# Kernel tuning notes

Measured on AMD Instinct MI355X. Metric: run time of the kernel, lower is better.

## Reference

```python
import jax, jax.numpy as jnp
import numpy as np

B, S, H, NH = 1, 2048, 2048, 16
HD = H // NH
EPS = 1e-5
NEG = jnp.finfo(jnp.float32).min


def _alibi_slopes(n_heads):
    # standard Bloom alibi slopes (n_heads power of 2)
    start = 2.0 ** (-(2.0 ** -(np.log2(n_heads) - 3)))
    return start * (start ** np.arange(n_heads))


def setup_inputs() -> dict:
    key = jax.random.key(0)
    ks = jax.random.split(key, 10)
    s = 0.02
    hidden_states = jax.random.normal(ks[0], (B, S, H), jnp.float32)
    # causal mask: True = masked (future positions)
    causal = ~jnp.tril(jnp.ones((S, S), dtype=bool))
    attention_mask = causal[None, None, :, :]  # [1,1,S,S]
    # alibi bias [B*NH, 1, S]
    slopes = jnp.asarray(_alibi_slopes(NH), jnp.float32)  # [NH]
    pos = jnp.arange(S, dtype=jnp.float32)
    alibi = (slopes[:, None] * pos[None, :])[:, None, :]  # [NH,1,S]
    alibi = jnp.tile(alibi, (B, 1, 1))  # [B*NH,1,S]
    return {
        "hidden_states": hidden_states,
        "attention_mask": attention_mask,
        "alibi": alibi,
        "head_mask": 0,
        "ln1_g": jnp.ones((H,), jnp.float32),
        "ln1_b": jnp.zeros((H,), jnp.float32),
        "qkv_w": jax.random.normal(ks[1], (3 * H, H), jnp.float32) * s,
        "qkv_b": jnp.zeros((3 * H,), jnp.float32),
        "dense_w": jax.random.normal(ks[2], (H, H), jnp.float32) * s,
        "dense_b": jnp.zeros((H,), jnp.float32),
        "ln2_g": jnp.ones((H,), jnp.float32),
        "ln2_b": jnp.zeros((H,), jnp.float32),
        "fc1_w": jax.random.normal(ks[3], (4 * H, H), jnp.float32) * s,
        "fc1_b": jnp.zeros((4 * H,), jnp.float32),
        "fc2_w": jax.random.normal(ks[4], (H, 4 * H), jnp.float32) * s,
        "fc2_b": jnp.zeros((H,), jnp.float32),
    }


def _ln(x, g, b):
    mu = jnp.mean(x, axis=-1, keepdims=True)
    var = jnp.mean(jnp.square(x - mu), axis=-1, keepdims=True)
    return (x - mu) * jax.lax.rsqrt(var + EPS) * g + b


def _gelu(x):
    # Bloom tanh-approx GELU
    return x * 0.5 * (1.0 + jnp.tanh(0.79788456 * x * (1.0 + 0.044715 * x * x)))


def reference(hidden_states, attention_mask, alibi, head_mask,
              ln1_g, ln1_b, qkv_w, qkv_b, dense_w, dense_b,
              ln2_g, ln2_b, fc1_w, fc1_b, fc2_w, fc2_b):
    b, s, h = hidden_states.shape
    x = _ln(hidden_states, ln1_g, ln1_b)
    residual = hidden_states  # apply_residual_connection_post_layernorm=False

    qkv = x @ qkv_w.T + qkv_b                      # [b,s,3H]
    qkv = qkv.reshape(b, s, NH, 3, HD)             # per-head interleaved
    q, k, v = qkv[..., 0, :], qkv[..., 1, :], qkv[..., 2, :]  # [b,s,nh,hd]

    inv = 1.0 / jnp.sqrt(jnp.float32(HD))
    scores = jnp.einsum('bqnd,bknd->bnqk', q, k) * inv  # [b,nh,s,s]
    scores = scores + alibi.reshape(b, NH, 1, s)
    scores = jnp.where(attention_mask, NEG, scores)
    w = jax.nn.softmax(scores, axis=-1)
    # head_mask == 0 -> falsy in original; no head masking applied
    ctx = jnp.einsum('bnqk,bknd->bqnd', w, v).reshape(b, s, h)
    attn_out = ctx @ dense_w.T + dense_b + residual

    y = _ln(attn_out, ln2_g, ln2_b)
    residual2 = attn_out
    hdn = _gelu(y @ fc1_w.T + fc1_b)
    out = hdn @ fc2_w.T + fc2_b + residual2
    return out
```

## Files before the change

kernel.cpp:

```cpp
#include <hip/hip_runtime.h>
#include <hip/hip_bf16.h>

#define SQ 2048
#define HH 2048
#define NHEAD 16
#define HD 128
#define QKVW (NHEAD*3*HD)

typedef __attribute__((ext_vector_type(8))) short bf16x8;
typedef __attribute__((ext_vector_type(4))) float f32x4;
typedef __attribute__((ext_vector_type(16))) float f32x16;

__device__ inline unsigned short f2bf(float f) {
    union { float f; unsigned u; } x; x.f = f;
    unsigned r = x.u + 0x7FFFu + ((x.u >> 16) & 1u);
    return (unsigned short)(r >> 16);
}

__device__ inline unsigned pack_bf2(float a, float b) {
    return (unsigned)f2bf(a) | ((unsigned)f2bf(b) << 16);
}

__device__ inline float gelu_f(float x) {
    float x3 = x * (1.f + 0.044715f * x * x);
    return 0.5f * x * (1.f + tanhf(0.79788456f * x3));
}

__device__ inline void gld16(void* lds, const void* g) {
    __builtin_amdgcn_global_load_lds(
        (__attribute__((address_space(1))) void*)(g),
        (__attribute__((address_space(3))) void*)(lds), 16, 0, 0);
}

__global__ __launch_bounds__(256) void cvt_kernel(
    const float* __restrict__ in, unsigned short* __restrict__ out, int n4)
{
    int i = blockIdx.x * blockDim.x + threadIdx.x;
    int stride = gridDim.x * blockDim.x;
    for (; i < n4; i += stride) {
        float4 f = ((const float4*)in)[i];
        ushort4 o;
        o.x = f2bf(f.x); o.y = f2bf(f.y); o.z = f2bf(f.z); o.w = f2bf(f.w);
        ((ushort4*)out)[i] = o;
    }
}

__global__ __launch_bounds__(256) void ln_kernel(
    const float* __restrict__ in, const float* __restrict__ g,
    const float* __restrict__ b, unsigned short* __restrict__ out)
{
    int row = blockIdx.x;
    int t = threadIdx.x, lane = t & 63, wid = t >> 6;
    const float4* rp = (const float4*)(in + (size_t)row * HH);
    float4 v0 = rp[t], v1 = rp[t + 256];
    float s  = v0.x + v0.y + v0.z + v0.w + v1.x + v1.y + v1.z + v1.w;
    float ss = v0.x*v0.x + v0.y*v0.y + v0.z*v0.z + v0.w*v0.w
             + v1.x*v1.x + v1.y*v1.y + v1.z*v1.z + v1.w*v1.w;
    #pragma unroll
    for (int o = 32; o; o >>= 1) { s += __shfl_down(s, o); ss += __shfl_down(ss, o); }
    __shared__ float r0[4], r1[4];
    if (lane == 0) { r0[wid] = s; r1[wid] = ss; }
    __syncthreads();
    s  = r0[0] + r0[1] + r0[2] + r0[3];
    ss = r1[0] + r1[1] + r1[2] + r1[3];
    float mu = s * (1.f / HH);
    float var = ss * (1.f / HH) - mu * mu;
    float rs = rsqrtf(var + 1e-5f);
    float4 g0 = ((const float4*)g)[t], g1 = ((const float4*)g)[t + 256];
    float4 b0 = ((const float4*)b)[t], b1 = ((const float4*)b)[t + 256];
    ushort4 o0, o1;
    o0.x = f2bf((v0.x - mu) * rs * g0.x + b0.x);
    o0.y = f2bf((v0.y - mu) * rs * g0.y + b0.y);
    o0.z = f2bf((v0.z - mu) * rs * g0.z + b0.z);
    o0.w = f2bf((v0.w - mu) * rs * g0.w + b0.w);
    o1.x = f2bf((v1.x - mu) * rs * g1.x + b1.x);
    o1.y = f2bf((v1.y - mu) * rs * g1.y + b1.y);
    o1.z = f2bf((v1.z - mu) * rs * g1.z + b1.z);
    o1.w = f2bf((v1.w - mu) * rs * g1.w + b1.w);
    ushort4* op = (ushort4*)(out + (size_t)row * HH);
    op[t] = o0; op[t + 256] = o1;
}

template<int NP>
__global__ __launch_bounds__(256) void reduceN_kernel(
    const float* __restrict__ p0, const float* __restrict__ p1,
    const float* __restrict__ p2, const float* __restrict__ p3,
    const float* __restrict__ res, const float* __restrict__ bias,
    float* __restrict__ out, int n4, int nc4m1)
{
    int i = blockIdx.x * blockDim.x + threadIdx.x;
    int st = gridDim.x * blockDim.x;
    for (; i < n4; i += st) {
        float4 a = ((const float4*)p0)[i];
        float4 b = ((const float4*)p1)[i];
        float4 r = ((const float4*)res)[i];
        float4 bv = ((const float4*)bias)[i & nc4m1];
        float4 o;
        o.x = a.x + b.x + r.x + bv.x;
        o.y = a.y + b.y + r.y + bv.y;
        o.z = a.z + b.z + r.z + bv.z;
        o.w = a.w + b.w + r.w + bv.w;
        if (NP >= 3) {
            float4 c = ((const float4*)p2)[i];
            o.x += c.x; o.y += c.y; o.z += c.z; o.w += c.w;
        }
        if (NP >= 4) {
            float4 d = ((const float4*)p3)[i];
            o.x += d.x; o.y += d.y; o.z += d.z; o.w += d.w;
        }
        ((float4*)out)[i] = o;
    }
}


template<int MODE, int GELU_ON>
__global__ __launch_bounds__(256, 4) void gemm128(
    const unsigned short* __restrict__ A, const unsigned short* __restrict__ B,
    const float* __restrict__ bias, void* __restrict__ outp,
    unsigned short* __restrict__ vtb, void* __restrict__ outp_hi,
    int N, int lda, int ldb, int kLen, int Ktot, int CH, int CW)
{
    __shared__ __align__(16) unsigned short Asm[2][128][32];
    __shared__ __align__(16) unsigned short Bsm[2][128][32];

    int t = threadIdx.x, lane = t & 63, wid = t >> 6;
    int lo = lane & 15, hi = lane >> 4;
    int wr = wid >> 1, wc = wid & 1;

    int id = (blockIdx.z * gridDim.y + blockIdx.y) * gridDim.x + blockIdx.x;
    int xcd = id & 7, local = id >> 3;
    int cgx = gridDim.x / CW;
    int cr = xcd / cgx, cc = xcd - cr * cgx;
    int lr = local / CW, lc = local - lr * CW;
    int R  = cr * CH + lr;
    int bn = cc * CW + lc;
    int bm = R % gridDim.y;
    int bz = R / gridDim.y;
    int m0 = bm * 128, n0 = bn * 128;
    int kstart = bz * kLen;
    int rem = Ktot - kstart;
    int nt = ((rem < kLen) ? rem : kLen) >> 5;

    int rS = t >> 2, cS = t & 3;
    int sc0_ = (cS ^ (rS & 3)) << 3;
    const unsigned short* Ab = A + (size_t)m0 * lda + kstart;
    const unsigned short* Bb = B + (size_t)n0 * ldb + kstart;
    const unsigned short* Asrc0 = Ab + (size_t)rS * lda + sc0_;
    const unsigned short* Asrc1 = Ab + (size_t)(64 + rS) * lda + sc0_;
    const unsigned short* Bsrc0 = Bb + (size_t)rS * ldb + sc0_;
    const unsigned short* Bsrc1 = Bb + (size_t)(64 + rS) * ldb + sc0_;

    gld16(&Asm[0][wid * 16][0], Asrc0);
    gld16(&Asm[0][64 + wid * 16][0], Asrc1);
    gld16(&Bsm[0][wid * 16][0], Bsrc0);
    gld16(&Bsm[0][64 + wid * 16][0], Bsrc1);
    __syncthreads();

    f32x4 acc[4][4] = {};
    for (int u = 0; u < nt; u++) {
        int buf = u & 1, nbuf = buf ^ 1;
        int t1 = ((u + 1 < nt) ? u + 1 : nt - 1) * 32;
        gld16(&Asm[nbuf][wid * 16][0], Asrc0 + t1);
        gld16(&Asm[nbuf][64 + wid * 16][0], Asrc1 + t1);
        gld16(&Bsm[nbuf][wid * 16][0], Bsrc0 + t1);
        gld16(&Bsm[nbuf][64 + wid * 16][0], Bsrc1 + t1);
        __builtin_amdgcn_s_setprio(1);
        {
            bf16x8 af[4], bfr[4];
            #pragma unroll
            for (int i = 0; i < 4; i++) {
                int r = wr * 64 + i * 16 + lo;
                af[i] = *(const bf16x8*)&Asm[buf][r][(hi ^ (r & 3)) << 3];
            }
            #pragma unroll
            for (int c = 0; c < 4; c++) {
                int r = wc * 64 + c * 16 + lo;
                bfr[c] = *(const bf16x8*)&Bsm[buf][r][(hi ^ (r & 3)) << 3];
            }
            #pragma unroll
            for (int i = 0; i < 4; i++)
                #pragma unroll
                for (int c = 0; c < 4; c++)
                    acc[i][c] = __builtin_amdgcn_mfma_f32_16x16x32_bf16(
                        bfr[c], af[i], acc[i][c], 0, 0, 0);
        }
        __builtin_amdgcn_s_setprio(0);
        __syncthreads();
    }

    if (MODE == 0) {
        float* po;
        if (bz == 0)      po = (float*)outp;
        else if (bz == 1) po = (float*)outp + (size_t)SQ * N;
        else if (bz == 2) po = (float*)outp_hi;
        else              po = (float*)vtb;
        #pragma unroll
        for (int i = 0; i < 4; i++) {
            int gr = m0 + wr * 64 + i * 16 + lo;
            #pragma unroll
            for (int c = 0; c < 4; c++) {
                int gc = n0 + wc * 64 + c * 16 + hi * 4;
                *(f32x4*)&po[(size_t)gr * N + gc] = acc[i][c];
            }
        }
    } else if (MODE == 1) {
        unsigned short* op = (unsigned short*)outp;
        #pragma unroll
        for (int i = 0; i < 4; i++) {
            int gr = m0 + wr * 64 + i * 16 + lo;
            #pragma unroll
            for (int c = 0; c < 4; c++) {
                int gc = n0 + wc * 64 + c * 16 + hi * 4;
                float4 bi = *(const float4*)&bias[gc];
                float v0 = acc[i][c][0] + bi.x, v1 = acc[i][c][1] + bi.y;
                float v2 = acc[i][c][2] + bi.z, v3 = acc[i][c][3] + bi.w;
                if (GELU_ON) { v0 = gelu_f(v0); v1 = gelu_f(v1); v2 = gelu_f(v2); v3 = gelu_f(v3); }
                ushort4 o; o.x = f2bf(v0); o.y = f2bf(v1); o.z = f2bf(v2); o.w = f2bf(v3);
                *(ushort4*)&op[(size_t)gr * N + gc] = o;
            }
        }
    } else {
        unsigned short* op = (unsigned short*)outp;
        int head = n0 / 384;
        int cat = (n0 >> 7) % 3;
        #pragma unroll
        for (int i = 0; i < 4; i++) {
            int gr = m0 + wr * 64 + i * 16 + lo;
            #pragma unroll
            for (int c = 0; c < 4; c++) {
                int gc = n0 + wc * 64 + c * 16 + hi * 4;
                float4 bi = *(const float4*)&bias[gc];
                float v0 = acc[i][c][0] + bi.x, v1 = acc[i][c][1] + bi.y;
                float v2 = acc[i][c][2] + bi.z, v3 = acc[i][c][3] + bi.w;
                if (cat == 2) {
                    int d = wc * 64 + c * 16 + hi * 4;
                    unsigned short* vp = vtb + (size_t)(head * HD + d) * SQ + gr;
                    vp[0]      = f2bf(v0);
                    vp[SQ]     = f2bf(v1);
                    vp[2 * SQ] = f2bf(v2);
                    vp[3 * SQ] = f2bf(v3);
                } else {
                    ushort4 o; o.x = f2bf(v0); o.y = f2bf(v1); o.z = f2bf(v2); o.w = f2bf(v3);
                    *(ushort4*)&op[(size_t)gr * N + gc] = o;
                }
            }
        }
    }
}

__global__ __launch_bounds__(128) void attn_kernel(
    const unsigned short* __restrict__ qkvB,
    const unsigned short* __restrict__ vtb,
    unsigned short* __restrict__ ctx)
{
    int w = blockIdx.x;
    int lid = (w & 7) * 64 + (w >> 3);
    int n = lid >> 5, qt = lid & 31;
    int t = threadIdx.x, lane = t & 63, wid = t >> 6;
    int l32 = lane & 31, h2 = lane >> 5;
    int q0 = qt * 64, qg = q0 + wid * 32 + l32;

    __shared__ __align__(16) unsigned short Ks[64][128];
    __shared__ __align__(16) unsigned short Vt[128][64];

    bf16x8 qf[8];
    const unsigned short* qp = qkvB + (size_t)qg * QKVW + n * 384 + h2 * 8;
    #pragma unroll
    for (int d8 = 0; d8 < 8; d8++)
        qf[d8] = *(const bf16x8*)(qp + d8 * 16);

    const float slope = exp2f(-0.5f * (float)(n + 1));
    const float inv = 0.08838834764831845f;
    float m = -INFINITY, lsum = 0.f;
    f32x16 ao[4] = {};

    int krow = lane >> 4, kch = lane & 15;
    int vrow = lane >> 3, vch = lane & 7;
    const unsigned short* kb_ = qkvB + n * 384 + 128;
    const unsigned short* vb_ = vtb + (size_t)n * HD * SQ;
    const char* ksb = (const char*)&Ks[0][0];
    const char* vsb = (const char*)&Vt[0][0];

    int nkb = qt + 1;
    for (int kb = 0; kb < nkb; kb++) {
        int k0 = kb * 64;
        __syncthreads();
        #pragma unroll
        for (int s = 0; s < 8; s++) {
            int r = wid * 32 + s * 4 + krow;
            gld16(&Ks[wid * 32 + s * 4][0],
                  kb_ + (size_t)(k0 + r) * QKVW + ((kch ^ (r & 7)) << 3));
            int dd = wid * 64 + s * 8 + vrow;
            gld16(&Vt[wid * 64 + s * 8][0],
                  vb_ + (size_t)dd * SQ + k0 + ((vch ^ (dd & 7)) << 3));
        }
        __syncthreads();

        f32x16 sc0 = {}, sc1 = {};
        #pragma unroll
        for (int d8 = 0; d8 < 8; d8++) {
            int ch = ((d8 * 2 + h2) ^ (l32 & 7)) << 4;
            bf16x8 kf0 = *(const bf16x8*)(ksb + l32 * 256 + ch);
            bf16x8 kf1 = *(const bf16x8*)(ksb + (32 + l32) * 256 + ch);
            sc0 = __builtin_amdgcn_mfma_f32_32x32x16_bf16(kf0, qf[d8], sc0, 0, 0, 0);
            sc1 = __builtin_amdgcn_mfma_f32_32x32x16_bf16(kf1, qf[d8], sc1, 0, 0, 0);
        }

        float tmax = -INFINITY;
        int last = (kb == nkb - 1);
        #pragma unroll
        for (int r = 0; r < 16; r++) {
            int kl = (r & 3) + 8 * (r >> 2) + 4 * h2;
            float s0 = sc0[r] * inv + slope * (float)(k0 + kl);
            float s1 = sc1[r] * inv + slope * (float)(k0 + 32 + kl);
            if (last) {
                if (k0 + kl > qg) s0 = -INFINITY;
                if (k0 + 32 + kl > qg) s1 = -INFINITY;
            }
            sc0[r] = s0; sc1[r] = s1;
            tmax = fmaxf(tmax, fmaxf(s0, s1));
        }
        tmax = fmaxf(tmax, __shfl_xor(tmax, 32));
        if (!__all(tmax <= m + 8.f)) {
            float mnew = fmaxf(m, tmax);
            float sca = __expf(m - mnew);
            m = mnew;
            lsum *= sca;
            #pragma unroll
            for (int db = 0; db < 4; db++)
                #pragma unroll
                for (int e = 0; e < 16; e++) ao[db][e] *= sca;
        }
        float psum = 0.f;
        #pragma unroll
        for (int r = 0; r < 16; r++) {
            sc0[r] = __expf(sc0[r] - m); psum += sc0[r];
            sc1[r] = __expf(sc1[r] - m); psum += sc1[r];
        }
        psum += __shfl_xor(psum, 32);
        lsum += psum;

        #pragma unroll
        for (int kstep = 0; kstep < 4; kstep++) {
            const int ks1 = kstep & 1;
            float a0, a1, a2, a3, b0, b1, b2, b3;
            if (kstep < 2) {
                a0 = sc0[8*ks1+0]; a1 = sc0[8*ks1+1]; a2 = sc0[8*ks1+2]; a3 = sc0[8*ks1+3];
                b0 = sc0[8*ks1+4]; b1 = sc0[8*ks1+5]; b2 = sc0[8*ks1+6]; b3 = sc0[8*ks1+7];
            } else {
                a0 = sc1[8*ks1+0]; a1 = sc1[8*ks1+1]; a2 = sc1[8*ks1+2]; a3 = sc1[8*ks1+3];
                b0 = sc1[8*ks1+4]; b1 = sc1[8*ks1+5]; b2 = sc1[8*ks1+6]; b3 = sc1[8*ks1+7];
            }
            unsigned ku0 = pack_bf2(h2 ? b0 : a0, h2 ? b1 : a1);
            unsigned ku1 = pack_bf2(h2 ? b2 : a2, h2 ? b3 : a3);
            unsigned su0 = pack_bf2(h2 ? a0 : b0, h2 ? a1 : b1);
            unsigned su1 = pack_bf2(h2 ? a2 : b2, h2 ? a3 : b3);
            unsigned r0 = (unsigned)__shfl_xor((int)su0, 32);
            unsigned r1 = (unsigned)__shfl_xor((int)su1, 32);
            union { int4 i; bf16x8 v; } u;
            u.i.x = h2 ? (int)r0  : (int)ku0;
            u.i.y = h2 ? (int)r1  : (int)ku1;
            u.i.z = h2 ? (int)ku0 : (int)r0;
            u.i.w = h2 ? (int)ku1 : (int)r1;
            bf16x8 pf = u.v;
            int ch = ((kstep * 2 + h2) ^ (l32 & 7)) << 4;
            #pragma unroll
            for (int db = 0; db < 4; db++) {
                bf16x8 vf = *(const bf16x8*)(vsb + (db * 32 + l32) * 128 + ch);
                ao[db] = __builtin_amdgcn_mfma_f32_32x32x16_bf16(vf, pf, ao[db], 0, 0, 0);
            }
        }
    }

    float rl = 1.f / lsum;
    #pragma unroll
    for (int db = 0; db < 4; db++)
        #pragma unroll
        for (int g = 0; g < 4; g++) {
            ushort4 o;
            o.x = f2bf(ao[db][g*4+0] * rl);
            o.y = f2bf(ao[db][g*4+1] * rl);
            o.z = f2bf(ao[db][g*4+2] * rl);
            o.w = f2bf(ao[db][g*4+3] * rl);
            *(ushort4*)(ctx + (size_t)qg * HH + n * HD + db * 32 + g * 8 + h2 * 4) = o;
        }
}

extern "C" void kernel_launch(void* const* d_in, const int* in_sizes, int n_in,
                              void* d_out, int out_size, void* d_ws, size_t ws_size,
                              hipStream_t stream) {
    const float* hs    = (const float*)d_in[0];
    const float* ln1g  = (const float*)d_in[4];
    const float* ln1b  = (const float*)d_in[5];
    const float* qkvw  = (const float*)d_in[6];
    const float* qkvb  = (const float*)d_in[7];
    const float* dw    = (const float*)d_in[8];
    const float* db    = (const float*)d_in[9];
    const float* ln2g  = (const float*)d_in[10];
    const float* ln2b  = (const float*)d_in[11];
    const float* f1w   = (const float*)d_in[12];
    const float* f1b   = (const float*)d_in[13];
    const float* f2w   = (const float*)d_in[14];
    const float* f2b   = (const float*)d_in[15];
    float* out = (float*)d_out;

    char* ws = (char*)d_ws;
    size_t off = 0;
    auto alloc = [&](size_t nbytes) {
        void* p = ws + off; off += (nbytes + 255) & ~(size_t)255; return p;
    };
    unsigned short* xbf  = (unsigned short*)alloc((size_t)SQ * HH * 2);
    unsigned short* qkvB = (unsigned short*)alloc((size_t)SQ * QKVW * 2);
    unsigned short* vtB  = (unsigned short*)alloc((size_t)NHEAD * HD * SQ * 2);
    unsigned short* ctx  = (unsigned short*)alloc((size_t)SQ * HH * 2);
    float*          attn = (float*)alloc((size_t)SQ * HH * 4);
    unsigned short* y    = (unsigned short*)alloc((size_t)SQ * HH * 2);
    unsigned short* hdn  = (unsigned short*)alloc((size_t)SQ * 4 * HH * 2);
    unsigned short* wbuf = (unsigned short*)alloc((size_t)4 * HH * HH * 2);

    const size_t PQ = (size_t)SQ * HH;
    float* part = (float*)ws;

    ln_kernel<<<SQ, 256, 0, stream>>>(hs, ln1g, ln1b, xbf);

    cvt_kernel<<<2048, 256, 0, stream>>>(qkvw, wbuf, QKVW * HH / 4);
    gemm128<2, 0><<<dim3(QKVW / 128, SQ / 128, 1), 256, 0, stream>>>(
        xbf, wbuf, qkvb, qkvB, vtB, nullptr, QKVW, HH, HH, HH, HH, 8, 12);

    attn_kernel<<<512, 128, 0, stream>>>(qkvB, vtB, ctx);

    cvt_kernel<<<1024, 256, 0, stream>>>(dw, wbuf, HH * HH / 4);
    gemm128<0, 0><<<dim3(HH / 128, SQ / 128, 4), 256, 0, stream>>>(
        ctx, wbuf, nullptr, part, (unsigned short*)((float*)hdn + PQ), hdn,
        HH, HH, HH, HH / 4, HH, 16, 8);
    reduceN_kernel<4><<<2048, 256, 0, stream>>>(
        part, part + PQ, (float*)hdn, (float*)hdn + PQ, hs, db, attn, SQ * HH / 4, HH / 4 - 1);

    ln_kernel<<<SQ, 256, 0, stream>>>(attn, ln2g, ln2b, y);

    cvt_kernel<<<2048, 256, 0, stream>>>(f1w, wbuf, 4 * HH * HH / 4);
    gemm128<1, 1><<<dim3(4 * HH / 128, SQ / 128, 1), 256, 0, stream>>>(
        y, wbuf, f1b, hdn, nullptr, nullptr, 4 * HH, HH, HH, HH, HH, 8, 16);

    cvt_kernel<<<2048, 256, 0, stream>>>(f2w, wbuf, 4 * HH * HH / 4);
    gemm128<0, 0><<<dim3(HH / 128, SQ / 128, 3), 256, 0, stream>>>(
        hdn, wbuf, nullptr, part, nullptr, part + 2 * PQ,
        HH, 4 * HH, 4 * HH, 2752, 4 * HH, 12, 8);
    reduceN_kernel<3><<<2048, 256, 0, stream>>>(
        part, part + PQ, part + 2 * PQ, nullptr, attn, f2b, out, SQ * HH / 4, HH / 4 - 1);
}
```

Baseline: 446.2 us.

## Use 256x256-tile 1024-thread GEMM for MLP layers and change LDS swizzle

Adds a gemm1024 kernel that uses 256x256 output tiles with 16 waves per block, and switches the FC1 and FC2 GEMMs to it. FC2 moves from a 3-way to a 4-way split-K, with the fourth partial written into the output buffer and reduced in place. The LDS XOR swizzle in both GEMMs now keys on (row>>1)&3 instead of row&3, to cut bank conflicts on the fragment reads. Larger tiles give more operand reuse per block, at the cost of fewer blocks and possibly lower occupancy, since launch_bounds(1024,4) is unlikely to hold with 64 KB of LDS per block.

Result: no change. 444.2 us (-0.4%).

```diff
diff --git a/kernel.cpp b/kernel.cpp
--- a/kernel.cpp
+++ b/kernel.cpp
@@ -112,7 +112,6 @@
     }
 }
 
-
 template<int MODE, int GELU_ON>
 __global__ __launch_bounds__(256, 4) void gemm128(
     const unsigned short* __restrict__ A, const unsigned short* __restrict__ B,
@@ -142,13 +141,14 @@
     int nt = ((rem < kLen) ? rem : kLen) >> 5;
 
     int rS = t >> 2, cS = t & 3;
-    int sc0_ = (cS ^ (rS & 3)) << 3;
+    int scA0 = (cS ^ ((rS >> 1) & 3)) << 3;
+    int scA1 = (cS ^ (((64 + rS) >> 1) & 3)) << 3;
     const unsigned short* Ab = A + (size_t)m0 * lda + kstart;
     const unsigned short* Bb = B + (size_t)n0 * ldb + kstart;
-    const unsigned short* Asrc0 = Ab + (size_t)rS * lda + sc0_;
-    const unsigned short* Asrc1 = Ab + (size_t)(64 + rS) * lda + sc0_;
-    const unsigned short* Bsrc0 = Bb + (size_t)rS * ldb + sc0_;
-    const unsigned short* Bsrc1 = Bb + (size_t)(64 + rS) * ldb + sc0_;
+    const unsigned short* Asrc0 = Ab + (size_t)rS * lda + scA0;
+    const unsigned short* Asrc1 = Ab + (size_t)(64 + rS) * lda + scA1;
+    const unsigned short* Bsrc0 = Bb + (size_t)rS * ldb + scA0;
+    const unsigned short* Bsrc1 = Bb + (size_t)(64 + rS) * ldb + scA1;
 
     gld16(&Asm[0][wid * 16][0], Asrc0);
     gld16(&Asm[0][64 + wid * 16][0], Asrc1);
@@ -170,12 +170,12 @@
             #pragma unroll
             for (int i = 0; i < 4; i++) {
                 int r = wr * 64 + i * 16 + lo;
-                af[i] = *(const bf16x8*)&Asm[buf][r][(hi ^ (r & 3)) << 3];
+                af[i] = *(const bf16x8*)&Asm[buf][r][(hi ^ ((r >> 1) & 3)) << 3];
             }
             #pragma unroll
             for (int c = 0; c < 4; c++) {
                 int r = wc * 64 + c * 16 + lo;
-                bfr[c] = *(const bf16x8*)&Bsm[buf][r][(hi ^ (r & 3)) << 3];
+                bfr[c] = *(const bf16x8*)&Bsm[buf][r][(hi ^ ((r >> 1) & 3)) << 3];
             }
             #pragma unroll
             for (int i = 0; i < 4; i++)
@@ -243,6 +243,104 @@
                     ushort4 o; o.x = f2bf(v0); o.y = f2bf(v1); o.z = f2bf(v2); o.w = f2bf(v3);
                     *(ushort4*)&op[(size_t)gr * N + gc] = o;
                 }
+            }
+        }
+    }
+}
+
+template<int MODE, int GELU_ON>
+__global__ __launch_bounds__(1024, 4) void gemm1024(
+    const unsigned short* __restrict__ A, const unsigned short* __restrict__ B,
+    const float* __restrict__ bias, void* __restrict__ outp,
+    void* __restrict__ outp_hi,
+    int N, int lda, int ldb, int kLen, int Ktot, int CH, int CW)
+{
+    __shared__ __align__(16) unsigned short Asm[2][256][32];
+    __shared__ __align__(16) unsigned short Bsm[2][256][32];
+
+    int t = threadIdx.x, lane = t & 63, wid = t >> 6;
+    int lo = lane & 15, hi = lane >> 4;
+    int wr = wid >> 2, wc = wid & 3;
+
+    int id = (blockIdx.z * gridDim.y + blockIdx.y) * gridDim.x + blockIdx.x;
+    int xcd = id & 7, local = id >> 3;
+    int cgx = gridDim.x / CW;
+    int cr = xcd / cgx, cc = xcd - cr * cgx;
+    int lr = local / CW, lc = local - lr * CW;
+    int R  = cr * CH + lr;
+    int bn = cc * CW + lc;
+    int bm = R % gridDim.y;
+    int bz = R / gridDim.y;
+    int m0 = bm * 256, n0 = bn * 256;
+    int kstart = bz * kLen;
+    int rem = Ktot - kstart;
+    int nt = ((rem < kLen) ? rem : kLen) >> 5;
+
+    int rS = t >> 2, cS = t & 3;
+    int scS = (cS ^ ((rS >> 1) & 3)) << 3;
+    const unsigned short* Asrc = A + (size_t)(m0 + rS) * lda + kstart + scS;
+    const unsigned short* Bsrc = B + (size_t)(n0 + rS) * ldb + kstart + scS;
+
+    gld16(&Asm[0][wid * 16][0], Asrc);
+    gld16(&Bsm[0][wid * 16][0], Bsrc);
+    __syncthreads();
+
+    f32x4 acc[4][4] = {};
+    for (int u = 0; u < nt; u++) {
+        int buf = u & 1, nbuf = buf ^ 1;
+        int t1 = ((u + 1 < nt) ? u + 1 : nt - 1) * 32;
+        gld16(&Asm[nbuf][wid * 16][0], Asrc + t1);
+        gld16(&Bsm[nbuf][wid * 16][0], Bsrc + t1);
+        __builtin_amdgcn_s_setprio(1);
+        {
+            bf16x8 af[4], bfr[4];
+            #pragma unroll
+            for (int i = 0; i < 4; i++) {
+                int r = wr * 64 + i * 16 + lo;
+                af[i] = *(const bf16x8*)&Asm[buf][r][(hi ^ ((r >> 1) & 3)) << 3];
+            }
+            #pragma unroll
+            for (int c = 0; c < 4; c++) {
+                int r = wc * 64 + c * 16 + lo;
+                bfr[c] = *(const bf16x8*)&Bsm[buf][r][(hi ^ ((r >> 1) & 3)) << 3];
+            }
+            #pragma unroll
+            for (int i = 0; i < 4; i++)
+                #pragma unroll
+                for (int c = 0; c < 4; c++)
+                    acc[i][c] = __builtin_amdgcn_mfma_f32_16x16x32_bf16(
+                        bfr[c], af[i], acc[i][c], 0, 0, 0);
+        }
+        __builtin_amdgcn_s_setprio(0);
+        __syncthreads();
+    }
+
+    if (MODE == 0) {
+        float* po = (bz < 3) ? (float*)outp + (size_t)bz * SQ * N
+                             : (float*)outp_hi;
+        #pragma unroll
+        for (int i = 0; i < 4; i++) {
+            int gr = m0 + wr * 64 + i * 16 + lo;
+            #pragma unroll
+            for (int c = 0; c < 4; c++) {
+                int gc = n0 + wc * 64 + c * 16 + hi * 4;
+                *(f32x4*)&po[(size_t)gr * N + gc] = acc[i][c];
+            }
+        }
+    } else {
+        unsigned short* op = (unsigned short*)outp;
+        #pragma unroll
+        for (int i = 0; i < 4; i++) {
+            int gr = m0 + wr * 64 + i * 16 + lo;
+            #pragma unroll
+            for (int c = 0; c < 4; c++) {
+                int gc = n0 + wc * 64 + c * 16 + hi * 4;
+                float4 bi = *(const float4*)&bias[gc];
+                float v0 = acc[i][c][0] + bi.x, v1 = acc[i][c][1] + bi.y;
+                float v2 = acc[i][c][2] + bi.z, v3 = acc[i][c][3] + bi.w;
+                if (GELU_ON) { v0 = gelu_f(v0); v1 = gelu_f(v1); v2 = gelu_f(v2); v3 = gelu_f(v3); }
+                ushort4 o; o.x = f2bf(v0); o.y = f2bf(v1); o.z = f2bf(v2); o.w = f2bf(v3);
+                *(ushort4*)&op[(size_t)gr * N + gc] = o;
             }
         }
     }
@@ -439,13 +537,12 @@
     ln_kernel<<<SQ, 256, 0, stream>>>(attn, ln2g, ln2b, y);
 
     cvt_kernel<<<2048, 256, 0, stream>>>(f1w, wbuf, 4 * HH * HH / 4);
-    gemm128<1, 1><<<dim3(4 * HH / 128, SQ / 128, 1), 256, 0, stream>>>(
-        y, wbuf, f1b, hdn, nullptr, nullptr, 4 * HH, HH, HH, HH, HH, 8, 16);
+    gemm1024<1, 1><<<dim3(4 * HH / 256, SQ / 256, 1), 1024, 0, stream>>>(
+        y, wbuf, f1b, hdn, nullptr, 4 * HH, HH, HH, HH, HH, 4, 8);
 
     cvt_kernel<<<2048, 256, 0, stream>>>(f2w, wbuf, 4 * HH * HH / 4);
-    gemm128<0, 0><<<dim3(HH / 128, SQ / 128, 3), 256, 0, stream>>>(
-        hdn, wbuf, nullptr, part, nullptr, part + 2 * PQ,
-        HH, 4 * HH, 4 * HH, 2752, 4 * HH, 12, 8);
-    reduceN_kernel<3><<<2048, 256, 0, stream>>>(
-        part, part + PQ, part + 2 * PQ, nullptr, attn, f2b, out, SQ * HH / 4, HH / 4 - 1);
-}
+    gemm1024<0, 0><<<dim3(HH / 256, SQ / 256, 4), 1024, 0, stream>>>(
+        hdn, wbuf, nullptr, part, out, HH, 4 * HH, 4 * HH, HH, 4 * HH, 8, 4);
+    reduceN_kernel<4><<<2048, 256, 0, stream>>>(
+        part, part + PQ, part + 2 * PQ, out, attn, f2b, out, SQ * HH / 4, HH / 4 - 1);
+}
```

## Switch GEMMs to 256x256 tiles with 1024-thread blocks and K=64 steps

Applied to the files above, without the earlier changes.

Replaces the 128x128, 256-thread GEMM with a 256x256 output tile computed by 16 waves, a K-step of 64 with an 8-way XOR swizzle in LDS, and retuned grid and chunking parameters. Each block reuses more data per tile, which cuts redundant global and L2 traffic for the A and B panels. The fc2 split-K changes from 3 to 4 chunks, with the fourth partial written into the output buffer and reduced in place. The cost is fewer blocks per GEMM, 128 KB of LDS per block that limits occupancy, and a larger wave count for each barrier to synchronise.

New measurement: 415.7 us. 1.07x faster.

```diff
diff --git a/kernel.cpp b/kernel.cpp
--- a/kernel.cpp
+++ b/kernel.cpp
@@ -112,20 +112,20 @@
     }
 }
 
-
 template<int MODE, int GELU_ON>
-__global__ __launch_bounds__(256, 4) void gemm128(
+__global__ __launch_bounds__(1024, 4) void gemm1024(
     const unsigned short* __restrict__ A, const unsigned short* __restrict__ B,
     const float* __restrict__ bias, void* __restrict__ outp,
     unsigned short* __restrict__ vtb, void* __restrict__ outp_hi,
+    void* __restrict__ outp_hi2,
     int N, int lda, int ldb, int kLen, int Ktot, int CH, int CW)
 {
-    __shared__ __align__(16) unsigned short Asm[2][128][32];
-    __shared__ __align__(16) unsigned short Bsm[2][128][32];
+    __shared__ __align__(16) unsigned short Asm[2][256][64];
+    __shared__ __align__(16) unsigned short Bsm[2][256][64];
 
     int t = threadIdx.x, lane = t & 63, wid = t >> 6;
     int lo = lane & 15, hi = lane >> 4;
-    int wr = wid >> 1, wc = wid & 1;
+    int wr = wid >> 2, wc = wid & 3;
 
     int id = (blockIdx.z * gridDim.y + blockIdx.y) * gridDim.x + blockIdx.x;
     int xcd = id & 7, local = id >> 3;
@@ -136,46 +136,46 @@
     int bn = cc * CW + lc;
     int bm = R % gridDim.y;
     int bz = R / gridDim.y;
-    int m0 = bm * 128, n0 = bn * 128;
+    int m0 = bm * 256, n0 = bn * 256;
     int kstart = bz * kLen;
     int rem = Ktot - kstart;
-    int nt = ((rem < kLen) ? rem : kLen) >> 5;
-
-    int rS = t >> 2, cS = t & 3;
-    int sc0_ = (cS ^ (rS & 3)) << 3;
-    const unsigned short* Ab = A + (size_t)m0 * lda + kstart;
-    const unsigned short* Bb = B + (size_t)n0 * ldb + kstart;
-    const unsigned short* Asrc0 = Ab + (size_t)rS * lda + sc0_;
-    const unsigned short* Asrc1 = Ab + (size_t)(64 + rS) * lda + sc0_;
-    const unsigned short* Bsrc0 = Bb + (size_t)rS * ldb + sc0_;
-    const unsigned short* Bsrc1 = Bb + (size_t)(64 + rS) * ldb + sc0_;
-
-    gld16(&Asm[0][wid * 16][0], Asrc0);
-    gld16(&Asm[0][64 + wid * 16][0], Asrc1);
-    gld16(&Bsm[0][wid * 16][0], Bsrc0);
-    gld16(&Bsm[0][64 + wid * 16][0], Bsrc1);
+    int nt = ((rem < kLen) ? rem : kLen) >> 6;
+
+    int rS = t >> 3, cS = t & 7;
+    int scS = (cS ^ (rS & 7)) << 3;
+    const unsigned short* Asrc0 = A + (size_t)(m0 + rS) * lda + kstart + scS;
+    const unsigned short* Asrc1 = A + (size_t)(m0 + 128 + rS) * lda + kstart + scS;
+    const unsigned short* Bsrc0 = B + (size_t)(n0 + rS) * ldb + kstart + scS;
+    const unsigned short* Bsrc1 = B + (size_t)(n0 + 128 + rS) * ldb + kstart + scS;
+
+    gld16(&Asm[0][wid * 8][0], Asrc0);
+    gld16(&Asm[0][128 + wid * 8][0], Asrc1);
+    gld16(&Bsm[0][wid * 8][0], Bsrc0);
+    gld16(&Bsm[0][128 + wid * 8][0], Bsrc1);
     __syncthreads();
 
     f32x4 acc[4][4] = {};
     for (int u = 0; u < nt; u++) {
         int buf = u & 1, nbuf = buf ^ 1;
-        int t1 = ((u + 1 < nt) ? u + 1 : nt - 1) * 32;
-        gld16(&Asm[nbuf][wid * 16][0], Asrc0 + t1);
-        gld16(&Asm[nbuf][64 + wid * 16][0], Asrc1 + t1);
-        gld16(&Bsm[nbuf][wid * 16][0], Bsrc0 + t1);
-        gld16(&Bsm[nbuf][64 + wid * 16][0], Bsrc1 + t1);
+        int t1 = ((u + 1 < nt) ? u + 1 : nt - 1) * 64;
+        gld16(&Asm[nbuf][wid * 8][0], Asrc0 + t1);
+        gld16(&Asm[nbuf][128 + wid * 8][0], Asrc1 + t1);
+        gld16(&Bsm[nbuf][wid * 8][0], Bsrc0 + t1);
+        gld16(&Bsm[nbuf][128 + wid * 8][0], Bsrc1 + t1);
         __builtin_amdgcn_s_setprio(1);
-        {
+        #pragma unroll
+        for (int ks = 0; ks < 2; ks++) {
+            int g = ks * 4 + hi;
             bf16x8 af[4], bfr[4];
             #pragma unroll
             for (int i = 0; i < 4; i++) {
                 int r = wr * 64 + i * 16 + lo;
-                af[i] = *(const bf16x8*)&Asm[buf][r][(hi ^ (r & 3)) << 3];
+                af[i] = *(const bf16x8*)&Asm[buf][r][(g ^ (r & 7)) << 3];
             }
             #pragma unroll
             for (int c = 0; c < 4; c++) {
                 int r = wc * 64 + c * 16 + lo;
-                bfr[c] = *(const bf16x8*)&Bsm[buf][r][(hi ^ (r & 3)) << 3];
+                bfr[c] = *(const bf16x8*)&Bsm[buf][r][(g ^ (r & 7)) << 3];
             }
             #pragma unroll
             for (int i = 0; i < 4; i++)
@@ -193,7 +193,7 @@
         if (bz == 0)      po = (float*)outp;
         else if (bz == 1) po = (float*)outp + (size_t)SQ * N;
         else if (bz == 2) po = (float*)outp_hi;
-        else              po = (float*)vtb;
+        else              po = (float*)outp_hi2;
         #pragma unroll
         for (int i = 0; i < 4; i++) {
             int gr = m0 + wr * 64 + i * 16 + lo;
@@ -221,19 +221,19 @@
         }
     } else {
         unsigned short* op = (unsigned short*)outp;
-        int head = n0 / 384;
-        int cat = (n0 >> 7) % 3;
         #pragma unroll
         for (int i = 0; i < 4; i++) {
             int gr = m0 + wr * 64 + i * 16 + lo;
             #pragma unroll
             for (int c = 0; c < 4; c++) {
                 int gc = n0 + wc * 64 + c * 16 + hi * 4;
+                int head = gc / 384;
+                int within = gc - head * 384;
                 float4 bi = *(const float4*)&bias[gc];
                 float v0 = acc[i][c][0] + bi.x, v1 = acc[i][c][1] + bi.y;
                 float v2 = acc[i][c][2] + bi.z, v3 = acc[i][c][3] + bi.w;
-                if (cat == 2) {
-                    int d = wc * 64 + c * 16 + hi * 4;
+                if (within >= 256) {
+                    int d = within - 256;
                     unsigned short* vp = vtb + (size_t)(head * HD + d) * SQ + gr;
                     vp[0]      = f2bf(v0);
                     vp[SQ]     = f2bf(v1);
@@ -424,28 +424,28 @@
     ln_kernel<<<SQ, 256, 0, stream>>>(hs, ln1g, ln1b, xbf);
 
     cvt_kernel<<<2048, 256, 0, stream>>>(qkvw, wbuf, QKVW * HH / 4);
-    gemm128<2, 0><<<dim3(QKVW / 128, SQ / 128, 1), 256, 0, stream>>>(
-        xbf, wbuf, qkvb, qkvB, vtB, nullptr, QKVW, HH, HH, HH, HH, 8, 12);
+    gemm1024<2, 0><<<dim3(QKVW / 256, SQ / 256, 1), 1024, 0, stream>>>(
+        xbf, wbuf, qkvb, qkvB, vtB, nullptr, nullptr, QKVW, HH, HH, HH, HH, 4, 6);
 
     attn_kernel<<<512, 128, 0, stream>>>(qkvB, vtB, ctx);
 
     cvt_kernel<<<1024, 256, 0, stream>>>(dw, wbuf, HH * HH / 4);
-    gemm128<0, 0><<<dim3(HH / 128, SQ / 128, 4), 256, 0, stream>>>(
-        ctx, wbuf, nullptr, part, (unsigned short*)((float*)hdn + PQ), hdn,
-        HH, HH, HH, HH / 4, HH, 16, 8);
+    gemm1024<0, 0><<<dim3(HH / 256, SQ / 256, 4), 1024, 0, stream>>>(
+        ctx, wbuf, nullptr, part, nullptr, hdn, (float*)hdn + PQ,
+        HH, HH, HH, HH / 4, HH, 8, 4);
     reduceN_kernel<4><<<2048, 256, 0, stream>>>(
         part, part + PQ, (float*)hdn, (float*)hdn + PQ, hs, db, attn, SQ * HH / 4, HH / 4 - 1);
 
     ln_kernel<<<SQ, 256, 0, stream>>>(attn, ln2g, ln2b, y);
 
     cvt_kernel<<<2048, 256, 0, stream>>>(f1w, wbuf, 4 * HH * HH / 4);
-    gemm128<1, 1><<<dim3(4 * HH / 128, SQ / 128, 1), 256, 0, stream>>>(
-        y, wbuf, f1b, hdn, nullptr, nullptr, 4 * HH, HH, HH, HH, HH, 8, 16);
+    gemm1024<1, 1><<<dim3(4 * HH / 256, SQ / 256, 1), 1024, 0, stream>>>(
+        y, wbuf, f1b, hdn, nullptr, nullptr, nullptr, 4 * HH, HH, HH, HH, HH, 4, 8);
 
     cvt_kernel<<<2048, 256, 0, stream>>>(f2w, wbuf, 4 * HH * HH / 4);
-    gemm128<0, 0><<<dim3(HH / 128, SQ / 128, 3), 256, 0, stream>>>(
-        hdn, wbuf, nullptr, part, nullptr, part + 2 * PQ,
-        HH, 4 * HH, 4 * HH, 2752, 4 * HH, 12, 8);
-    reduceN_kernel<3><<<2048, 256, 0, stream>>>(
-        part, part + PQ, part + 2 * PQ, nullptr, attn, f2b, out, SQ * HH / 4, HH / 4 - 1);
-}
+    gemm1024<0, 0><<<dim3(HH / 256, SQ / 256, 4), 1024, 0, stream>>>(
+        hdn, wbuf, nullptr, part, nullptr, part + 2 * PQ, out,
+        HH, 4 * HH, 4 * HH, HH, 4 * HH, 8, 4);
+    reduceN_kernel<4><<<2048, 256, 0, stream>>>(
+        part, part + PQ, part + 2 * PQ, out, attn, f2b, out, SQ * HH / 4, HH / 4 - 1);
+}
```
